# Kernel tuning notes

Measured on AMD Instinct MI355X. Metric: run time of the kernel, lower is better.

The kernel has to match this reference:

```python
import jax, jax.numpy as jnp
import numpy as np

B, S, H = 2, 2048, 1024
NH, HD = 16, 64  # num_heads, head_size


def setup_inputs() -> dict:
    key = jax.random.key(0)
    ks = jax.random.split(key, 8)
    return {
        "x": jax.random.normal(ks[0], (B, S, H), dtype=jnp.float32),
        "attn_mask": jax.random.randint(ks[1], (B, S, S), 0, 2, dtype=jnp.int32),
        "Wq": jax.random.normal(ks[2], (H, H), dtype=jnp.float32) * 0.02,
        "bq": jax.random.normal(ks[3], (H,), dtype=jnp.float32) * 0.02,
        "Wk": jax.random.normal(ks[4], (H, H), dtype=jnp.float32) * 0.02,
        "bk": jax.random.normal(ks[5], (H,), dtype=jnp.float32) * 0.02,
        "Wv": jax.random.normal(ks[6], (H, H), dtype=jnp.float32) * 0.02,
        "bv": jax.random.normal(ks[7], (H,), dtype=jnp.float32) * 0.02,
    }


def reference(x, attn_mask, Wq, bq, Wk, bk, Wv, bv):
    b, s, h = x.shape
    # QKV projections (self-attention: kv = attention_input)
    q = (jnp.einsum('bih,hx->bix', x, Wq) + bq).reshape(b, s, NH, HD)
    k = (jnp.einsum('bih,hx->bix', x, Wk) + bk).reshape(b, s, NH, HD)
    v = (jnp.einsum('bih,hx->bix', x, Wv) + bv).reshape(b, s, NH, HD)
    scale = 1.0 / (HD ** 0.5)
    # [B, NH, Sq, Skv] score matrix, additive mask, softmax
    attn_score = jnp.einsum('bind,bjnd->bnij', q, k) * scale
    adder = attn_mask.astype(jnp.float32)[:, None, :, :] * -10000.0
    attn_prob = jax.nn.softmax(attn_score + adder, axis=-1)
    # dropout is identity (training=False)
    attn_vec = jnp.einsum('bnij,bjnd->bind', attn_prob, v)
    return attn_vec.reshape(b, s, NH * HD)
```

## Files before the change

kernel.cpp:

```cpp
#include <hip/hip_runtime.h>
#include <hip/hip_bf16.h>
#include <math.h>


#define DI __device__ __forceinline__

typedef unsigned short u16;
typedef unsigned int u32;
typedef unsigned long long u64;
typedef __attribute__((ext_vector_type(8))) short bf16x8;
typedef __attribute__((ext_vector_type(4))) float f32x4;

constexpr int BB = 2, SS = 2048, HH = 1024, NHEAD = 16, HDIM = 64;

DI u16 f2bf(float f) {
  __hip_bfloat16 h = __float2bfloat16(f);
  union { __hip_bfloat16 h; u16 u; } c; c.h = h; return c.u;
}

DI void gload_lds16(const void* g, const void* l) {
  __builtin_amdgcn_global_load_lds(
      (const __attribute__((address_space(1))) u32*)(u64)g,
      (__attribute__((address_space(3))) u32*)(u32)(u64)l,
      16, 0, 0);
}

__global__ void prep(const float* __restrict__ x, u16* __restrict__ xb,
                     const float* __restrict__ Wq, const float* __restrict__ Wk,
                     const float* __restrict__ Wv, u16* __restrict__ WT,
                     const int* __restrict__ mask, u64* __restrict__ mb) {
  __shared__ u16 tile[64][65];
  const int bid = blockIdx.x;
  if (bid < 2048) {
    const size_t i = ((size_t)bid * 256 + threadIdx.x) * 8;
    float4 f0 = *(const float4*)(x + i);
    float4 f1 = *(const float4*)(x + i + 4);
    bf16x8 v;
    v[0] = (short)f2bf(f0.x); v[1] = (short)f2bf(f0.y);
    v[2] = (short)f2bf(f0.z); v[3] = (short)f2bf(f0.w);
    v[4] = (short)f2bf(f1.x); v[5] = (short)f2bf(f1.y);
    v[6] = (short)f2bf(f1.z); v[7] = (short)f2bf(f1.w);
    *(bf16x8*)(xb + i) = v;
  } else if (bid < 2816) {
    const int idx = bid - 2048;
    const int z = idx >> 8, rem = idx & 255;
    const int n0 = (rem & 15) * 64, k0 = (rem >> 4) * 64;
    const float* W = (z == 0) ? Wq : (z == 1) ? Wk : Wv;
    u16* Wt = WT + (size_t)z * HH * HH;
    for (int i = threadIdx.x; i < 64 * 64; i += 256) {
      int r = i >> 6, c = i & 63;
      tile[r][c] = f2bf(W[(size_t)(k0 + r) * HH + n0 + c]);
    }
    __syncthreads();
    for (int i = threadIdx.x; i < 64 * 64; i += 256) {
      int r = i >> 6, c = i & 63;
      Wt[(size_t)(n0 + r) * HH + k0 + c] = tile[c][r];
    }
  } else {
    const size_t idx = (size_t)(bid - 2816) * 256 + threadIdx.x;
    const int v = mask[idx];
    const u64 bal = __ballot(v != 0);
    if ((threadIdx.x & 63) == 0) mb[idx >> 6] = bal;
  }
}

__global__ __launch_bounds__(256) void qkv_gemm(
    const u16* __restrict__ X, const u16* __restrict__ WTall,
    const float* __restrict__ bq, const float* __restrict__ bk,
    const float* __restrict__ bv,
    u16* __restrict__ Qo, u16* __restrict__ Ko, u16* __restrict__ Vo) {
  __shared__ alignas(128) u16 As[128 * 64];
  __shared__ alignas(128) u16 Bs[128 * 64];

  const int bid = blockIdx.x;
  const int xcd = bid & 7;
  const int q = bid >> 3;
  const int xb = q & 7;
  const int sl = q >> 3;
  const int slice = sl * 8 + xcd;
  const int y = slice & 31, z = slice >> 5;

  const u16* Wt = WTall + (size_t)z * HH * HH;
  const float* bias = (z == 0) ? bq : (z == 1) ? bk : bv;
  u16* Out = (z == 0) ? Qo : (z == 1) ? Ko : Vo;
  const float oscale = (z == 0) ? 0.18033688011112042f : 1.0f;

  const int tid = threadIdx.x;
  const int lane = tid & 63;
  const int w = tid >> 6;
  const int wm = (w >> 1) * 64, wn = (w & 1) * 64;
  const int lr = lane & 15, lkg = lane >> 4;
  const int m0 = y * 128, n0 = xb * 128;

  u32 srow[4], scol[4];
#pragma unroll
  for (int i = 0; i < 4; ++i) {
    u32 f = i * 4096 + w * 1024 + lane * 16;
    u32 g = f ^ (((f >> 7) & 7) << 4);
    srow[i] = g >> 7;
    scol[i] = (g & 127) >> 1;
  }

  u32 aoff[4][2], boff[4][2];
#pragma unroll
  for (int mf = 0; mf < 4; ++mf)
#pragma unroll
    for (int ks = 0; ks < 2; ++ks) {
      int row = wm + mf * 16 + lr;
      aoff[mf][ks] = (u32)((row * 128 + ks * 64 + lkg * 16) ^ ((row & 7) << 4));
      row = wn + mf * 16 + lr;
      boff[mf][ks] = (u32)((row * 128 + ks * 64 + lkg * 16) ^ ((row & 7) << 4));
    }

  f32x4 acc[4][4];
#pragma unroll
  for (int i = 0; i < 4; ++i)
#pragma unroll
    for (int j = 0; j < 4; ++j) acc[i][j] = {0.f, 0.f, 0.f, 0.f};

  const u16* Xb2 = X + (size_t)m0 * HH;
  const u16* Wb = Wt + (size_t)n0 * HH;

  auto stage = [&](int kt) {
    const int k0 = kt * 64;
#pragma unroll
    for (int i = 0; i < 4; ++i) {
      gload_lds16(Xb2 + (size_t)srow[i] * HH + k0 + scol[i],
                  (const char*)As + i * 4096 + w * 1024);
      gload_lds16(Wb + (size_t)srow[i] * HH + k0 + scol[i],
                  (const char*)Bs + i * 4096 + w * 1024);
    }
  };

  stage(0);
  const int NT = HH / 64;
  for (int kt = 0; kt < NT; ++kt) {
    __syncthreads();
    bf16x8 a[2][4], bfr[2][4];
#pragma unroll
    for (int ks = 0; ks < 2; ++ks)
#pragma unroll
      for (int i = 0; i < 4; ++i) {
        a[ks][i] = *(const bf16x8*)((const char*)As + aoff[i][ks]);
        bfr[ks][i] = *(const bf16x8*)((const char*)Bs + boff[i][ks]);
      }
    __syncthreads();
    if (kt + 1 < NT) stage(kt + 1);
    __builtin_amdgcn_s_setprio(1);
#pragma unroll
    for (int ks = 0; ks < 2; ++ks)
#pragma unroll
      for (int mf = 0; mf < 4; ++mf)
#pragma unroll
        for (int nf = 0; nf < 4; ++nf)
          acc[mf][nf] = __builtin_amdgcn_mfma_f32_16x16x32_bf16(
              a[ks][mf], bfr[ks][nf], acc[mf][nf], 0, 0, 0);
    __builtin_amdgcn_s_setprio(0);
  }

  if (z < 2) {
#pragma unroll
    for (int mf = 0; mf < 4; ++mf)
#pragma unroll
      for (int nf = 0; nf < 4; ++nf) {
        const int gn = n0 + wn + nf * 16 + lr;
        const float bvv = bias[gn];
        const int nh = gn >> 6, hd = gn & 63;
#pragma unroll
        for (int r = 0; r < 4; ++r) {
          const int gm = m0 + wm + mf * 16 + lkg * 4 + r;
          const int bb = gm >> 11, ss = gm & 2047;
          const float v = (acc[mf][nf][r] + bvv) * oscale;
          Out[(((size_t)bb * NHEAD + nh) * SS + ss) * HDIM + hd] = f2bf(v);
        }
      }
  } else {
    char* Lw = (char*)As + w * 8192;
#pragma unroll
    for (int nf = 0; nf < 4; ++nf) {
      const int col = nf * 16 + lr;
      const float bvv = bias[(n0 + wn) + col];
#pragma unroll
      for (int mf = 0; mf < 4; ++mf) {
        union { u16 h[4]; u64 d; } pk;
#pragma unroll
        for (int r = 0; r < 4; ++r) pk.h[r] = f2bf(acc[mf][nf][r] + bvv);
        u32 byte = (u32)(col * 128 + mf * 32 + lkg * 8);
        byte ^= (u32)((col & 7) << 4);
        *(u64*)(Lw + byte) = pk.d;
      }
    }
    const int gm0 = m0 + wm;
    const int bb = gm0 >> 11, ss0 = gm0 & 2047;
    const int nh = (n0 + wn) >> 6;
    u16* Vbase = Out + ((size_t)(bb * NHEAD + nh) * HDIM) * SS + ss0;
#pragma unroll
    for (int it = 0; it < 8; ++it) {
      const int idx = it * 64 + lane;
      const int col = idx >> 3, sub = idx & 7;
      const u32 byte = (u32)(col * 128 + sub * 16) ^ (u32)((col & 7) << 4);
      const bf16x8 v = *(const bf16x8*)(Lw + byte);
      *(bf16x8*)(Vbase + (size_t)col * SS + sub * 8) = v;
    }
  }
}

__global__ __launch_bounds__(256) void attn(
    const u16* __restrict__ Q, const u16* __restrict__ K,
    const u16* __restrict__ Vt, const u64* __restrict__ mb,
    float* __restrict__ out) {
  __shared__ alignas(128) u16 Ks[64 * 64];
  __shared__ alignas(128) u16 Vs[64 * 64];
  __shared__ alignas(128) u16 Ps[4][16][72];

  const int f = blockIdx.x;
  const int xcd = f & 7, qt = (f >> 3) & 31, chi = f >> 8;
  const int c = xcd + 8 * chi;
  const int nh = c & 15, b = c >> 4;

  const int bnh = b * NHEAD + nh;
  const u16* Qh = Q + (size_t)bnh * SS * HDIM;
  const u16* Kh = K + (size_t)bnh * SS * HDIM;
  const u16* Vh = Vt + (size_t)bnh * HDIM * SS;
  const int q0 = qt * 64;

  const int tid = threadIdx.x, lane = tid & 63, w = tid >> 6;
  const int lr = lane & 15, lkg = lane >> 4;
  const int qrow_lane = q0 + w * 16 + lr;

  bf16x8 qf[2];
#pragma unroll
  for (int h = 0; h < 2; ++h)
    qf[h] = *(const bf16x8*)(Qh + (size_t)qrow_lane * HDIM + h * 32 + lkg * 8);

  u32 srow[2], scol[2];
#pragma unroll
  for (int i = 0; i < 2; ++i) {
    u32 fo = i * 4096 + w * 1024 + lane * 16;
    u32 g = fo ^ (((fo >> 7) & 7) << 4);
    srow[i] = g >> 7;
    scol[i] = (g & 127) >> 1;
  }

  auto stage = [&](int t) {
    const int kv0 = t * 64;
#pragma unroll
    for (int i = 0; i < 2; ++i) {
      gload_lds16(Kh + (size_t)(kv0 + srow[i]) * HDIM + scol[i],
                  (const char*)Ks + i * 4096 + w * 1024);
      gload_lds16(Vh + (size_t)srow[i] * SS + kv0 + scol[i],
                  (const char*)Vs + i * 4096 + w * 1024);
    }
  };

  u32 koff[4][2];
#pragma unroll
  for (int i = 0; i < 4; ++i)
#pragma unroll
    for (int h = 0; h < 2; ++h) {
      int row = i * 16 + lr;
      koff[i][h] = (u32)((row * 128 + h * 64 + lkg * 16) ^ ((row & 7) << 4));
    }

  bf16x8 ones;
#pragma unroll
  for (int j = 0; j < 8; ++j) ones[j] = (short)0x3F80;

  f32x4 oacc[4];
  f32x4 lacc = {0.f, 0.f, 0.f, 0.f};
#pragma unroll
  for (int n = 0; n < 4; ++n) oacc[n] = {0.f, 0.f, 0.f, 0.f};

  stage(0);
  const int NT = SS / 64;
  for (int t = 0; t < NT; ++t) {
    __syncthreads();

    const u64 sh =
        mb[((size_t)b * SS + qrow_lane) * (SS / 64) + t] >> (lkg * 4);
    const u32 w01 = (u32)sh, w23 = (u32)(sh >> 32);

    f32x4 sacc[4];
#pragma unroll
    for (int kvb = 0; kvb < 4; ++kvb) sacc[kvb] = {0.f, 0.f, 0.f, 0.f};
    __builtin_amdgcn_s_setprio(1);
#pragma unroll
    for (int kvb = 0; kvb < 4; ++kvb)
#pragma unroll
      for (int h = 0; h < 2; ++h) {
        const bf16x8 kf = *(const bf16x8*)((const char*)Ks + koff[kvb][h]);
        sacc[kvb] = __builtin_amdgcn_mfma_f32_16x16x32_bf16(
            kf, qf[h], sacc[kvb], 0, 0, 0);
      }
    __builtin_amdgcn_s_setprio(0);

#pragma unroll
    for (int kvb = 0; kvb < 4; ++kvb) {
      const u32 word = (kvb < 2) ? w01 : w23;
      const int sb = (kvb & 1) * 16;
      union { u16 h[4]; u64 d; } pk;
#pragma unroll
      for (int r = 0; r < 4; ++r) {
        float s = sacc[kvb][r];
        s = ((word >> (sb + r)) & 1u) ? -14000.0f : s;
        pk.h[r] = f2bf(__builtin_amdgcn_exp2f(s));
      }
      *(u64*)&Ps[w][lr][kvb * 16 + lkg * 4] = pk.d;
    }

    __builtin_amdgcn_s_setprio(1);
#pragma unroll
    for (int ks = 0; ks < 2; ++ks) {
      const bf16x8 pf = *(const bf16x8*)&Ps[w][lr][ks * 32 + lkg * 8];
#pragma unroll
      for (int n = 0; n < 4; ++n) {
        const bf16x8 vf = *(const bf16x8*)((const char*)Vs + koff[n][ks]);
        oacc[n] = __builtin_amdgcn_mfma_f32_16x16x32_bf16(
            pf, vf, oacc[n], 0, 0, 0);
      }
      lacc = __builtin_amdgcn_mfma_f32_16x16x32_bf16(pf, ones, lacc, 0, 0, 0);
    }
    __builtin_amdgcn_s_setprio(0);

    __syncthreads();
    if (t + 1 < NT) stage(t + 1);
  }

#pragma unroll
  for (int r = 0; r < 4; ++r) {
    const float rcp = 1.0f / lacc[r];
    const int qrow = q0 + w * 16 + lkg * 4 + r;
#pragma unroll
    for (int n = 0; n < 4; ++n)
      out[((size_t)b * SS + qrow) * HH + nh * HDIM + n * 16 + lr] =
          oacc[n][r] * rcp;
  }
}

extern "C" void kernel_launch(void* const* d_in, const int* in_sizes, int n_in,
                              void* d_out, int out_size, void* d_ws,
                              size_t ws_size, hipStream_t stream) {
  const float* x = (const float*)d_in[0];
  const int* mask = (const int*)d_in[1];
  const float* Wq = (const float*)d_in[2];
  const float* bq = (const float*)d_in[3];
  const float* Wk = (const float*)d_in[4];
  const float* bk = (const float*)d_in[5];
  const float* Wv = (const float*)d_in[6];
  const float* bv = (const float*)d_in[7];
  float* out = (float*)d_out;

  char* ws = (char*)d_ws;
  const size_t MB = 1024 * 1024;
  u16* Qw = (u16*)(ws + 0 * MB);
  u16* Kw = (u16*)(ws + 8 * MB);
  u16* Vtw = (u16*)(ws + 16 * MB);
  u64* mbp = (u64*)(ws + 24 * MB);
  u16* Xb = (u16*)d_out;
  u16* WT = (u16*)((char*)d_out + 8 * MB);

  prep<<<dim3(2048 + 768 + 32768), 256, 0, stream>>>(x, Xb, Wq, Wk, Wv, WT,
                                                     mask, mbp);
  qkv_gemm<<<dim3(768), 256, 0, stream>>>(Xb, WT, bq, bk, bv, Qw, Kw, Vtw);
  attn<<<dim3(NHEAD * (SS / 64) * BB), 256, 0, stream>>>(Qw, Kw, Vtw, mbp, out);
}
```

Before: 113.2 us.

## Split attention warps 2x2 over query rows and KV halves with LDS reduction

Each warp now covers 32 query rows and half of each 64-wide KV tile, where it previously covered 16 rows and the full tile. Every K and V fragment read from LDS therefore feeds two MFMAs, which halves LDS fragment traffic per MFMA. The two KV-half partial outputs and row sums are combined through shared memory in an epilogue with an extra barrier. This costs more registers (double accumulators and Q fragments) and adds the combine step.

```diff
diff --git a/kernel.cpp b/kernel.cpp
--- a/kernel.cpp
+++ b/kernel.cpp
@@ -209,9 +209,12 @@
     const u16* __restrict__ Q, const u16* __restrict__ K,
     const u16* __restrict__ Vt, const u64* __restrict__ mb,
     float* __restrict__ out) {
-  __shared__ alignas(128) u16 Ks[64 * 64];
-  __shared__ alignas(128) u16 Vs[64 * 64];
-  __shared__ alignas(128) u16 Ps[4][16][72];
+  __shared__ alignas(128) char smem[8192 + 8192 + 4 * 32 * 40 * 2];
+  u16* Ks = (u16*)smem;
+  u16* Vs = (u16*)(smem + 8192);
+  typedef u16 PsRow[32][40];
+  PsRow* Ps = (PsRow*)(smem + 16384);
+  float* cmb = (float*)smem;
 
   const int f = blockIdx.x;
   const int xcd = f & 7, qt = (f >> 3) & 31, chi = f >> 8;
@@ -225,13 +228,16 @@
   const int q0 = qt * 64;
 
   const int tid = threadIdx.x, lane = tid & 63, w = tid >> 6;
+  const int qh = w & 1, kh = w >> 1;
   const int lr = lane & 15, lkg = lane >> 4;
-  const int qrow_lane = q0 + w * 16 + lr;
-
-  bf16x8 qf[2];
-#pragma unroll
-  for (int h = 0; h < 2; ++h)
-    qf[h] = *(const bf16x8*)(Qh + (size_t)qrow_lane * HDIM + h * 32 + lkg * 8);
+
+  bf16x8 qf[2][2];
+#pragma unroll
+  for (int m = 0; m < 2; ++m)
+#pragma unroll
+    for (int h = 0; h < 2; ++h)
+      qf[m][h] = *(const bf16x8*)(Qh +
+          (size_t)(q0 + qh * 32 + m * 16 + lr) * HDIM + h * 32 + lkg * 8);
 
   u32 srow[2], scol[2];
 #pragma unroll
@@ -266,59 +272,79 @@
 #pragma unroll
   for (int j = 0; j < 8; ++j) ones[j] = (short)0x3F80;
 
-  f32x4 oacc[4];
-  f32x4 lacc = {0.f, 0.f, 0.f, 0.f};
-#pragma unroll
-  for (int n = 0; n < 4; ++n) oacc[n] = {0.f, 0.f, 0.f, 0.f};
+  f32x4 oacc[2][4];
+  f32x4 lacc[2];
+#pragma unroll
+  for (int m = 0; m < 2; ++m) {
+#pragma unroll
+    for (int n = 0; n < 4; ++n) oacc[m][n] = {0.f, 0.f, 0.f, 0.f};
+    lacc[m] = {0.f, 0.f, 0.f, 0.f};
+  }
 
   stage(0);
   const int NT = SS / 64;
   for (int t = 0; t < NT; ++t) {
     __syncthreads();
 
-    const u64 sh =
-        mb[((size_t)b * SS + qrow_lane) * (SS / 64) + t] >> (lkg * 4);
-    const u32 w01 = (u32)sh, w23 = (u32)(sh >> 32);
-
-    f32x4 sacc[4];
-#pragma unroll
-    for (int kvb = 0; kvb < 4; ++kvb) sacc[kvb] = {0.f, 0.f, 0.f, 0.f};
+    u32 mw[2];
+#pragma unroll
+    for (int m = 0; m < 2; ++m) {
+      const u64 word =
+          mb[((size_t)b * SS + (q0 + qh * 32 + m * 16 + lr)) * (SS / 64) + t];
+      mw[m] = (u32)(word >> (kh * 32 + lkg * 4));
+    }
+
+    f32x4 sacc[2][2];
+#pragma unroll
+    for (int m = 0; m < 2; ++m)
+#pragma unroll
+      for (int kvb = 0; kvb < 2; ++kvb) sacc[m][kvb] = {0.f, 0.f, 0.f, 0.f};
     __builtin_amdgcn_s_setprio(1);
 #pragma unroll
-    for (int kvb = 0; kvb < 4; ++kvb)
+    for (int kvb = 0; kvb < 2; ++kvb)
 #pragma unroll
       for (int h = 0; h < 2; ++h) {
-        const bf16x8 kf = *(const bf16x8*)((const char*)Ks + koff[kvb][h]);
-        sacc[kvb] = __builtin_amdgcn_mfma_f32_16x16x32_bf16(
-            kf, qf[h], sacc[kvb], 0, 0, 0);
+        const bf16x8 kf =
+            *(const bf16x8*)((const char*)Ks + koff[kh * 2 + kvb][h]);
+#pragma unroll
+        for (int m = 0; m < 2; ++m)
+          sacc[m][kvb] = __builtin_amdgcn_mfma_f32_16x16x32_bf16(
+              kf, qf[m][h], sacc[m][kvb], 0, 0, 0);
       }
     __builtin_amdgcn_s_setprio(0);
 
 #pragma unroll
-    for (int kvb = 0; kvb < 4; ++kvb) {
-      const u32 word = (kvb < 2) ? w01 : w23;
-      const int sb = (kvb & 1) * 16;
-      union { u16 h[4]; u64 d; } pk;
-#pragma unroll
-      for (int r = 0; r < 4; ++r) {
-        float s = sacc[kvb][r];
-        s = ((word >> (sb + r)) & 1u) ? -14000.0f : s;
-        pk.h[r] = f2bf(__builtin_amdgcn_exp2f(s));
-      }
-      *(u64*)&Ps[w][lr][kvb * 16 + lkg * 4] = pk.d;
-    }
+    for (int m = 0; m < 2; ++m)
+#pragma unroll
+      for (int kvb = 0; kvb < 2; ++kvb) {
+        union { u16 h[4]; u64 d; } pk;
+#pragma unroll
+        for (int r = 0; r < 4; ++r) {
+          float s = sacc[m][kvb][r];
+          s = ((mw[m] >> (kvb * 16 + r)) & 1u) ? -14000.0f : s;
+          pk.h[r] = f2bf(__builtin_amdgcn_exp2f(s));
+        }
+        *(u64*)&Ps[w][m * 16 + lr][kvb * 16 + lkg * 4] = pk.d;
+      }
 
     __builtin_amdgcn_s_setprio(1);
-#pragma unroll
-    for (int ks = 0; ks < 2; ++ks) {
-      const bf16x8 pf = *(const bf16x8*)&Ps[w][lr][ks * 32 + lkg * 8];
+    {
+      bf16x8 pf[2];
+#pragma unroll
+      for (int m = 0; m < 2; ++m)
+        pf[m] = *(const bf16x8*)&Ps[w][m * 16 + lr][lkg * 8];
 #pragma unroll
       for (int n = 0; n < 4; ++n) {
-        const bf16x8 vf = *(const bf16x8*)((const char*)Vs + koff[n][ks]);
-        oacc[n] = __builtin_amdgcn_mfma_f32_16x16x32_bf16(
-            pf, vf, oacc[n], 0, 0, 0);
-      }
-      lacc = __builtin_amdgcn_mfma_f32_16x16x32_bf16(pf, ones, lacc, 0, 0, 0);
+        const bf16x8 vf = *(const bf16x8*)((const char*)Vs + koff[n][kh]);
+#pragma unroll
+        for (int m = 0; m < 2; ++m)
+          oacc[m][n] = __builtin_amdgcn_mfma_f32_16x16x32_bf16(
+              pf[m], vf, oacc[m][n], 0, 0, 0);
+      }
+#pragma unroll
+      for (int m = 0; m < 2; ++m)
+        lacc[m] = __builtin_amdgcn_mfma_f32_16x16x32_bf16(
+            pf[m], ones, lacc[m], 0, 0, 0);
     }
     __builtin_amdgcn_s_setprio(0);
 
@@ -326,14 +352,37 @@
     if (t + 1 < NT) stage(t + 1);
   }
 
-#pragma unroll
-  for (int r = 0; r < 4; ++r) {
-    const float rcp = 1.0f / lacc[r];
-    const int qrow = q0 + w * 16 + lkg * 4 + r;
-#pragma unroll
-    for (int n = 0; n < 4; ++n)
-      out[((size_t)b * SS + qrow) * HH + nh * HDIM + n * 16 + lr] =
-          oacc[n][r] * rcp;
+  const int lid = qh * 64 + lane;
+  if (kh == 1) {
+#pragma unroll
+    for (int m = 0; m < 2; ++m) {
+#pragma unroll
+      for (int n = 0; n < 4; ++n)
+#pragma unroll
+        for (int r = 0; r < 4; ++r)
+          cmb[(m * 16 + n * 4 + r) * 128 + lid] = oacc[m][n][r];
+#pragma unroll
+      for (int r = 0; r < 4; ++r)
+        cmb[(32 + m * 4 + r) * 128 + lid] = lacc[m][r];
+    }
+  }
+  __syncthreads();
+  if (kh == 0) {
+#pragma unroll
+    for (int m = 0; m < 2; ++m)
+#pragma unroll
+      for (int r = 0; r < 4; ++r) {
+        const float l = lacc[m][r] + cmb[(32 + m * 4 + r) * 128 + lid];
+        const float rcp = 1.0f / l;
+        const int qrow = q0 + qh * 32 + m * 16 + lkg * 4 + r;
+#pragma unroll
+        for (int n = 0; n < 4; ++n) {
+          const float o =
+              oacc[m][n][r] + cmb[(m * 16 + n * 4 + r) * 128 + lid];
+          out[((size_t)b * SS + qrow) * HH + nh * HDIM + n * 16 + lr] =
+              o * rcp;
+        }
+      }
   }
 }
 
```

After: 153.7 us. +35.8%, slower.
